# Performance work log

Measured on AMD Instinct MI355X. Metric: run time of the kernel, lower is better.

Reference implementation:

```python
import jax, jax.numpy as jnp
import numpy as np

B, T, D, H, F = 256, 512, 200, 128, 128
LAM = 0.5


def _xavier(key, shape, gain=1.0):
    fan_in, fan_out = shape[0], shape[1]
    lim = gain * np.sqrt(6.0 / (fan_in + fan_out))
    return jax.random.uniform(key, shape, minval=-lim, maxval=lim, dtype=jnp.float32)


def setup_inputs() -> dict:
    key = jax.random.key(0)
    ks = jax.random.split(key, 32)
    inp = {
        "hrrp": jax.random.normal(ks[0], (B, T, D), jnp.float32),
        "amplitude_corr": jax.random.normal(ks[1], (B, T), jnp.float32),
        "phase_corr": jax.random.normal(ks[2], (B, T), jnp.float32),
        "rlos_delta": jax.random.normal(ks[3], (B, T, 2), jnp.float32),
        # TwoStageFusion params (weights stored [in, out])
        "f_amp_w": _xavier(ks[4], (1, F)), "f_amp_b": jnp.zeros((F,)),
        "f_ph_w": _xavier(ks[5], (1, F)), "f_ph_b": jnp.zeros((F,)),
        "f_gate_w": _xavier(ks[6], (2 * F, F)), "f_gate_b": jnp.zeros((F,)),
        "f_rlos_w1": _xavier(ks[7], (2, F)), "f_rlos_b1": jnp.zeros((F,)),
        "f_rlos_w2": _xavier(ks[8], (F, F)), "f_rlos_b2": jnp.zeros((F,)),
        "f_q_w": _xavier(ks[9], (F, F)), "f_q_b": jnp.zeros((F,)),
        "f_k_w": _xavier(ks[10], (F, F)), "f_k_b": jnp.zeros((F,)),
        "f_v_w": _xavier(ks[11], (F, F)), "f_v_b": jnp.zeros((F,)),
        "f_out_w": _xavier(ks[12], (F, F)), "f_out_b": jnp.zeros((F,)),
        # CGLSTM cell params; layer 0 has input_dim=D, layers 1-2 have input_dim=H
        "base_w0": _xavier(ks[13], (D + H, 4 * H)),
        "base_b0": jnp.zeros((4 * H,)).at[H:2 * H].set(1.0),
        "gam_w0": jnp.stack([_xavier(ks[14 + i], (F, H), gain=0.5) for i in range(4)]),
        "base_w12": jnp.stack([_xavier(ks[18 + l], (H + H, 4 * H)) for l in range(2)]),
        "base_b12": jnp.tile(jnp.zeros((4 * H,)).at[H:2 * H].set(1.0)[None], (2, 1)),
        "gam_w12": jnp.stack([jnp.stack([_xavier(ks[20 + 4 * l + i], (F, H), gain=0.5) for i in range(4)]) for l in range(2)]),
        "reg_w": _xavier(ks[28], (H, 2)), "reg_b": jnp.zeros((2,)),
    }
    return inp


def _cell(x, h, c, g, W, b, GW):
    # base linear over concat([h, x]) -> 4 gates; gamma-modulated
    z = jnp.concatenate([h, x], axis=-1) @ W + b
    bi, bf, bc, bo = jnp.split(z, 4, axis=-1)
    i = jax.nn.sigmoid(bi + g @ GW[0])
    f = jax.nn.sigmoid(bf - LAM * (g @ GW[1]))
    ch = jnp.tanh(bc + g @ GW[2])
    o = jax.nn.sigmoid(bo + g @ GW[3])
    c2 = f * c + i * ch
    h2 = o * jnp.tanh(c2)
    return h2, c2


def reference(hrrp, amplitude_corr, phase_corr, rlos_delta,
              f_amp_w, f_amp_b, f_ph_w, f_ph_b, f_gate_w, f_gate_b,
              f_rlos_w1, f_rlos_b1, f_rlos_w2, f_rlos_b2,
              f_q_w, f_q_b, f_k_w, f_k_b, f_v_w, f_v_b, f_out_w, f_out_b,
              base_w0, base_b0, gam_w0, base_w12, base_b12, gam_w12,
              reg_w, reg_b):
    # --- TwoStageFusion ---
    amp = jnp.tanh(amplitude_corr[..., None] @ f_amp_w + f_amp_b)    # [B,T,F]
    ph = jnp.tanh(phase_corr[..., None] @ f_ph_w + f_ph_b)           # [B,T,F]
    beta = jax.nn.sigmoid(jnp.concatenate([ph, amp], -1) @ f_gate_w + f_gate_b)
    corr = beta * ph + (1.0 - beta) * amp
    rl = jnp.tanh(jnp.tanh(rlos_delta @ f_rlos_w1 + f_rlos_b1) @ f_rlos_w2 + f_rlos_b2)
    q = corr @ f_q_w + f_q_b
    k = rl @ f_k_w + f_k_b
    v = rl @ f_v_w + f_v_b
    attn = jax.nn.sigmoid(jnp.sum(q * k, -1, keepdims=True) * (F ** -0.5))
    gamma = (attn * v) @ f_out_w + f_out_b                            # [B,T,F]

    # --- StackedCGLSTM: gamma_t at step t is gamma[:, t-1], zeros at t=0 ---
    gamma_sh = jnp.concatenate([jnp.zeros((gamma.shape[0], 1, gamma.shape[-1]), gamma.dtype),
                                gamma[:, :-1]], axis=1)
    xs = (jnp.swapaxes(hrrp, 0, 1), jnp.swapaxes(gamma_sh, 0, 1))     # [T,B,*]

    bsz = hrrp.shape[0]
    z = jnp.zeros((bsz, H), hrrp.dtype)
    init = ((z, z, z), (z, z, z))

    def step(carry, xt):
        x_t, g_t = xt
        hs, cs = carry
        inp = jnp.abs(x_t)
        h0, c0 = _cell(inp, hs[0], cs[0], g_t, base_w0, base_b0, gam_w0)
        h1, c1 = _cell(h0, hs[1], cs[1], g_t, base_w12[0], base_b12[0], gam_w12[0])
        h2, c2 = _cell(h1, hs[2], cs[2], g_t, base_w12[1], base_b12[1], gam_w12[1])
        return ((h0, h1, h2), (c0, c1, c2)), None

    (hs, _), _ = jax.lax.scan(step, init, xs)
    return hs[2] @ reg_w + reg_b                                      # [B,2]
```

## Files before the change

kernel.cpp:

```cpp
#include <hip/hip_runtime.h>

#define BB 256
#define TT 512
#define DD 200

__device__ __forceinline__ float bf2f(unsigned short u) {
    return __uint_as_float(((unsigned int)u) << 16);
}
__device__ __forceinline__ unsigned short f2bf(float f) {
    unsigned int u = __float_as_uint(f);
    u += 0x7FFFu + ((u >> 16) & 1u);
    return (unsigned short)(u >> 16);
}
__device__ __forceinline__ float sigm(float x) { return 1.0f / (1.0f + __expf(-x)); }
__device__ __forceinline__ float tanh_(float x) { return 1.0f - 2.0f / (__expf(2.0f * x) + 1.0f); }

typedef __bf16 bf16x8 __attribute__((ext_vector_type(8)));
typedef float  f32x4  __attribute__((ext_vector_type(4)));

#define GPAD 20

__device__ __forceinline__ void gll16(const unsigned short* g, unsigned short* l) {
    __builtin_amdgcn_global_load_lds(
        (const __attribute__((address_space(1))) unsigned int*)g,
        (__attribute__((address_space(3))) unsigned int*)l,
        16, 0, 0);
}

#define MAC16(ACCV, BASE, W) do { \
    const float4* _p4 = (const float4*)(BASE); \
    float4 _v0 = _p4[0], _v1 = _p4[1], _v2 = _p4[2], _v3 = _p4[3]; \
    ACCV[0]  = fmaf(_v0.x,(W),ACCV[0]);  ACCV[1]  = fmaf(_v0.y,(W),ACCV[1]); \
    ACCV[2]  = fmaf(_v0.z,(W),ACCV[2]);  ACCV[3]  = fmaf(_v0.w,(W),ACCV[3]); \
    ACCV[4]  = fmaf(_v1.x,(W),ACCV[4]);  ACCV[5]  = fmaf(_v1.y,(W),ACCV[5]); \
    ACCV[6]  = fmaf(_v1.z,(W),ACCV[6]);  ACCV[7]  = fmaf(_v1.w,(W),ACCV[7]); \
    ACCV[8]  = fmaf(_v2.x,(W),ACCV[8]);  ACCV[9]  = fmaf(_v2.y,(W),ACCV[9]); \
    ACCV[10] = fmaf(_v2.z,(W),ACCV[10]); ACCV[11] = fmaf(_v2.w,(W),ACCV[11]); \
    ACCV[12] = fmaf(_v3.x,(W),ACCV[12]); ACCV[13] = fmaf(_v3.y,(W),ACCV[13]); \
    ACCV[14] = fmaf(_v3.z,(W),ACCV[14]); ACCV[15] = fmaf(_v3.w,(W),ACCV[15]); \
} while (0)

#define MAC8(ACCV, BASE, W) do { \
    const float4* _p4 = (const float4*)(BASE); \
    float4 _v0 = _p4[0], _v1 = _p4[1]; \
    ACCV[0] = fmaf(_v0.x,(W),ACCV[0]); ACCV[1] = fmaf(_v0.y,(W),ACCV[1]); \
    ACCV[2] = fmaf(_v0.z,(W),ACCV[2]); ACCV[3] = fmaf(_v0.w,(W),ACCV[3]); \
    ACCV[4] = fmaf(_v1.x,(W),ACCV[4]); ACCV[5] = fmaf(_v1.y,(W),ACCV[5]); \
    ACCV[6] = fmaf(_v1.z,(W),ACCV[6]); ACCV[7] = fmaf(_v1.w,(W),ACCV[7]); \
} while (0)

#define MAC8_2(A1, A2, BASE, W1, W2) do { \
    const float4* _p4 = (const float4*)(BASE); \
    float4 _v0 = _p4[0], _v1 = _p4[1]; \
    A1[0] = fmaf(_v0.x,(W1),A1[0]); A2[0] = fmaf(_v0.x,(W2),A2[0]); \
    A1[1] = fmaf(_v0.y,(W1),A1[1]); A2[1] = fmaf(_v0.y,(W2),A2[1]); \
    A1[2] = fmaf(_v0.z,(W1),A1[2]); A2[2] = fmaf(_v0.z,(W2),A2[2]); \
    A1[3] = fmaf(_v0.w,(W1),A1[3]); A2[3] = fmaf(_v0.w,(W2),A2[3]); \
    A1[4] = fmaf(_v1.x,(W1),A1[4]); A2[4] = fmaf(_v1.x,(W2),A2[4]); \
    A1[5] = fmaf(_v1.y,(W1),A1[5]); A2[5] = fmaf(_v1.y,(W2),A2[5]); \
    A1[6] = fmaf(_v1.z,(W1),A1[6]); A2[6] = fmaf(_v1.z,(W2),A2[6]); \
    A1[7] = fmaf(_v1.w,(W1),A1[7]); A2[7] = fmaf(_v1.w,(W2),A2[7]); \
} while (0)

__global__ __launch_bounds__(256) void k_prep_b(
    const float* __restrict__ w0, const float* __restrict__ gw0,
    const float* __restrict__ w12, const float* __restrict__ gw12,
    unsigned short* __restrict__ b0t, unsigned short* __restrict__ b1t,
    unsigned short* __restrict__ b2t)
{
    const int n = blockIdx.x;
    const int gate = n >> 7, oo = n & 127;
    const float sgn = (gate == 1) ? -0.5f : 1.0f;
    for (int k = threadIdx.x; k < 1056; k += 256) {
        float w; int isLo;
        if (k < 672) {
            int blk = k / 224, col = k - blk * 224;
            w = (col < 200) ? w0[(size_t)(128 + col) * 512 + n] : 0.f;
            isLo = (blk == 1);
        } else {
            int kg = k - 672, blkg = kg >> 7, colg = kg & 127;
            w = sgn * gw0[(size_t)(gate * 128 + colg) * 128 + oo];
            isLo = (blkg == 1);
        }
        unsigned short hi = f2bf(w);
        b0t[(size_t)n * 1056 + k] = isLo ? f2bf(w - bf2f(hi)) : hi;
    }
    for (int l = 0; l < 2; ++l) {
        unsigned short* dst = l ? b2t : b1t;
        for (int k = threadIdx.x; k < 768; k += 256) {
            float w; int isLo;
            if (k < 384) {
                int blk = k >> 7, col = k & 127;
                w = w12[(size_t)(l * 256 + 128 + col) * 512 + n];
                isLo = (blk == 1);
            } else {
                int kg = k - 384, blkg = kg >> 7, colg = kg & 127;
                w = sgn * gw12[(size_t)((l * 4 + gate) * 128 + colg) * 128 + oo];
                isLo = (blkg == 1);
            }
            unsigned short hi = f2bf(w);
            dst[(size_t)n * 768 + k] = isLo ? f2bf(w - bf2f(hi)) : hi;
        }
    }
}

__global__ __launch_bounds__(128) void k_prep_fuse(
    const float* __restrict__ w_q, const float* __restrict__ b_q,
    const float* __restrict__ w_k, const float* __restrict__ b_k,
    const float* __restrict__ w_v, const float* __restrict__ b_v,
    const float* __restrict__ w_o,
    float* __restrict__ GT, float* __restrict__ WVO,
    float* __restrict__ e1, float* __restrict__ e2,
    float* __restrict__ e0, float* __restrict__ bvo)
{
    __shared__ float sk[128], sv[128];
    __shared__ float rtmp[8];
    const int i = blockIdx.x, f = threadIdx.x;
    sk[f] = w_k[(size_t)i * 128 + f];
    sv[f] = w_v[(size_t)i * 128 + f];
    __syncthreads();
    float g = 0.f, wv = 0.f;
    #pragma unroll 4
    for (int a = 0; a < 128; ++a) {
        g  = fmaf(w_q[(size_t)f * 128 + a], sk[a], g);
        wv = fmaf(sv[a], w_o[(size_t)a * 128 + f], wv);
    }
    GT[(size_t)i * 128 + f] = g;
    WVO[(size_t)i * 128 + f] = wv;
    float p1 = w_q[(size_t)i * 128 + f] * b_k[f];
    float p2 = sk[f] * b_q[f];
    #pragma unroll
    for (int sh = 32; sh > 0; sh >>= 1) {
        p1 += __shfl_xor(p1, sh, 64);
        p2 += __shfl_xor(p2, sh, 64);
    }
    if ((f & 63) == 0) { rtmp[(f >> 6) * 2] = p1; rtmp[(f >> 6) * 2 + 1] = p2; }
    __syncthreads();
    if (f == 0) { e1[i] = rtmp[0] + rtmp[2]; e2[i] = rtmp[1] + rtmp[3]; }
    if (i == 0) {
        float bw = 0.f;
        #pragma unroll 4
        for (int a = 0; a < 128; ++a) bw = fmaf(b_v[a], w_o[(size_t)a * 128 + f], bw);
        bvo[f] = bw;
        float p0 = b_q[f] * b_k[f];
        #pragma unroll
        for (int sh = 32; sh > 0; sh >>= 1) p0 += __shfl_xor(p0, sh, 64);
        if ((f & 63) == 0) rtmp[4 + (f >> 6)] = p0;
        __syncthreads();
        if (f == 0) e0[0] = rtmp[4] + rtmp[5];
    }
}

__global__ __launch_bounds__(256, 4) void k_gamma2(
    const float* __restrict__ ac, const float* __restrict__ pc,
    const float* __restrict__ rd,
    const float* __restrict__ w_amp, const float* __restrict__ b_amp,
    const float* __restrict__ w_ph,  const float* __restrict__ b_ph,
    const float* __restrict__ w_g,   const float* __restrict__ b_g,
    const float* __restrict__ w_r1,  const float* __restrict__ b_r1,
    const float* __restrict__ w_r2,  const float* __restrict__ b_r2,
    const float* __restrict__ GT,    const float* __restrict__ WVO,
    const float* __restrict__ e1,    const float* __restrict__ e2,
    const float* __restrict__ e0,    const float* __restrict__ bvo,
    const float* __restrict__ b_o,
    unsigned short* __restrict__ gsh, int segLen, int lgSeg, int tbase)
{
    __shared__ alignas(16) float catT[256][GPAD];
    __shared__ alignas(16) float rlT[128][GPAD];
    __shared__ float scin[4][16];
    __shared__ float red[2][2][8];

    const int tid = threadIdx.x;
    const int f = tid & 127;
    const int th = tid >> 7;
    const int t0 = th * 8;
    const int r0 = blockIdx.x * 16;
    const int b = r0 >> lgSeg;
    const int tl = r0 & (segLen - 1);
    const int tau0 = tbase + tl - 1;

    if (tid < 64) {
        int j = tid >> 4, tt = tid & 15;
        int tau = tau0 + tt; if (tau < 0) tau = 0;
        size_t tok = (size_t)b * TT + tau;
        float v;
        if (j == 0) v = ac[tok];
        else if (j == 1) v = pc[tok];
        else v = rd[tok * 2 + (j - 2)];
        scin[j][tt] = v;
    }
    const float wa = w_amp[f], ba = b_amp[f];
    const float wp = w_ph[f],  bpv = b_ph[f];
    const float w1a = w_r1[f], w1b = w_r1[128 + f];
    const float br1 = b_r1[f], br2v = b_r2[f];
    const float bg = b_g[f];
    __syncthreads();

    float ph8[8], am8[8];
    #pragma unroll
    for (int t = 0; t < 8; ++t) {
        float a = scin[0][t0 + t], p = scin[1][t0 + t];
        float r0v = scin[2][t0 + t], r1v = scin[3][t0 + t];
        float phv = tanh_(fmaf(p, wp, bpv));
        float amv = tanh_(fmaf(a, wa, ba));
        ph8[t] = phv; am8[t] = amv;
        catT[f][t0 + t] = phv;
        catT[128 + f][t0 + t] = amv;
        rlT[f][t0 + t] = tanh_(fmaf(r1v, w1b, fmaf(r0v, w1a, br1)));
    }
    __syncthreads();

    float bacc[8], racc[8];
    #pragma unroll
    for (int t = 0; t < 8; ++t) { bacc[t] = 0.f; racc[t] = 0.f; }
    #pragma unroll 2
    for (int i = 0; i < 128; ++i) {
        float wg1 = w_g[i * 128 + f];
        float wg2 = w_g[(128 + i) * 128 + f];
        float wr  = w_r2[i * 128 + f];
        MAC8(bacc, &catT[i][t0], wg1);
        MAC8(bacc, &catT[128 + i][t0], wg2);
        MAC8(racc, &rlT[i][t0], wr);
    }
    float corr8[8], rl8[8];
    #pragma unroll
    for (int t = 0; t < 8; ++t) {
        float beta = sigm(bacc[t] + bg);
        corr8[t] = fmaf(beta, ph8[t] - am8[t], am8[t]);
        rl8[t] = tanh_(racc[t] + br2v);
    }
    __syncthreads();
    #pragma unroll
    for (int t = 0; t < 8; ++t) rlT[f][t0 + t] = rl8[t];
    __syncthreads();

    float uacc[8], voacc[8];
    #pragma unroll
    for (int t = 0; t < 8; ++t) { uacc[t] = 0.f; voacc[t] = 0.f; }
    #pragma unroll 2
    for (int i = 0; i < 128; ++i) {
        float wu = GT[i * 128 + f];
        float wv = WVO[i * 128 + f];
        MAC8_2(uacc, voacc, &rlT[i][t0], wu, wv);
    }

    const int lane = tid & 63, wv2 = (tid >> 6) & 1;
    const float e1f = e1[f], e2f = e2[f], e0v = e0[0];
    #pragma unroll
    for (int t = 0; t < 8; ++t) {
        float pdot = fmaf(corr8[t], uacc[t] + e1f, rl8[t] * e2f);
        #pragma unroll
        for (int sh = 32; sh > 0; sh >>= 1) pdot += __shfl_xor(pdot, sh, 64);
        if (lane == 0) red[th][wv2][t] = pdot;
    }
    __syncthreads();
    const float bvof = bvo[f], bof = b_o[f];
    #pragma unroll
    for (int t = 0; t < 8; ++t) {
        float attn = sigm((red[th][0][t] + red[th][1][t] + e0v) * 0.088388347648318447f);
        float g = fmaf(attn, voacc[t] + bvof, bof);
        if (tau0 + t0 + t < 0) g = 0.f;
        unsigned short hi = f2bf(g);
        gsh[(size_t)(r0 + t0 + t) * 256 + f] = hi;
        gsh[(size_t)(r0 + t0 + t) * 256 + 128 + f] = f2bf(g - bf2f(hi));
    }
}

__global__ __launch_bounds__(128) void k_gamma(
    const float* __restrict__ ac, const float* __restrict__ pc,
    const float* __restrict__ rd,
    const float* __restrict__ w_amp, const float* __restrict__ b_amp,
    const float* __restrict__ w_ph,  const float* __restrict__ b_ph,
    const float* __restrict__ w_g,   const float* __restrict__ b_g,
    const float* __restrict__ w_r1,  const float* __restrict__ b_r1,
    const float* __restrict__ w_r2,  const float* __restrict__ b_r2,
    const float* __restrict__ w_q,   const float* __restrict__ b_q,
    const float* __restrict__ w_k,   const float* __restrict__ b_k,
    const float* __restrict__ w_v,   const float* __restrict__ b_v,
    const float* __restrict__ w_o,   const float* __restrict__ b_o,
    unsigned short* __restrict__ gsh, int segLen, int lgSeg, int tbase)
{
    __shared__ alignas(16) float catT[256][GPAD];
    __shared__ alignas(16) float rlT[128][GPAD];
    __shared__ alignas(16) float avT[128][GPAD];
    __shared__ float scin[4][16];
    __shared__ float red[2][16];

    const int f = threadIdx.x;
    const int r0 = blockIdx.x * 16;
    const int b = r0 >> lgSeg;
    const int tl = r0 & (segLen - 1);
    const int tau0 = tbase + tl - 1;

    if (f < 64) {
        int j = f >> 4, tt = f & 15;
        int tau = tau0 + tt; if (tau < 0) tau = 0;
        size_t tok = (size_t)b * TT + tau;
        float v;
        if (j == 0) v = ac[tok];
        else if (j == 1) v = pc[tok];
        else v = rd[tok * 2 + (j - 2)];
        scin[j][tt] = v;
    }
    const float wa = w_amp[f], ba = b_amp[f];
    const float wp = w_ph[f],  bpv = b_ph[f];
    const float w1a = w_r1[f], w1b = w_r1[128 + f];
    const float br1 = b_r1[f], br2 = b_r2[f];
    const float bg = b_g[f];
    const float bqv = b_q[f], bkv = b_k[f];
    const float bvv = b_v[f], bov = b_o[f];
    __syncthreads();

    float ph16[16], am16[16];
    #pragma unroll
    for (int t = 0; t < 16; ++t) {
        float a = scin[0][t], p = scin[1][t], r0v = scin[2][t], r1v = scin[3][t];
        float phv = tanh_(fmaf(p, wp, bpv));
        float amv = tanh_(fmaf(a, wa, ba));
        ph16[t] = phv; am16[t] = amv;
        catT[f][t] = phv;
        catT[128 + f][t] = amv;
        rlT[f][t] = tanh_(fmaf(r1v, w1b, fmaf(r0v, w1a, br1)));
    }
    __syncthreads();

    float bacc[16], racc[16];
    #pragma unroll
    for (int t = 0; t < 16; ++t) { bacc[t] = 0.f; racc[t] = 0.f; }
    #pragma unroll 2
    for (int i = 0; i < 128; ++i) {
        float wg1 = w_g[i * 128 + f];
        float wg2 = w_g[(128 + i) * 128 + f];
        float wr  = w_r2[i * 128 + f];
        MAC16(bacc, &catT[i][0], wg1);
        MAC16(bacc, &catT[128 + i][0], wg2);
        MAC16(racc, &rlT[i][0], wr);
    }
    float corr16[16], rl16[16];
    #pragma unroll
    for (int t = 0; t < 16; ++t) {
        float beta = sigm(bacc[t] + bg);
        corr16[t] = fmaf(beta, ph16[t] - am16[t], am16[t]);
        rl16[t] = tanh_(racc[t] + br2);
    }
    __syncthreads();
    #pragma unroll
    for (int t = 0; t < 16; ++t) { catT[f][t] = corr16[t]; rlT[f][t] = rl16[t]; }
    __syncthreads();

    float qa[16], ka[16], va[16];
    #pragma unroll
    for (int t = 0; t < 16; ++t) { qa[t] = 0.f; ka[t] = 0.f; va[t] = 0.f; }
    #pragma unroll 2
    for (int i = 0; i < 128; ++i) {
        float wq = w_q[i * 128 + f];
        float wk = w_k[i * 128 + f];
        float wv = w_v[i * 128 + f];
        MAC16(qa, &catT[i][0], wq);
        MAC16(ka, &rlT[i][0], wk);
        MAC16(va, &rlT[i][0], wv);
    }
    const int lane = f & 63, wvi = f >> 6;
    #pragma unroll
    for (int t = 0; t < 16; ++t) {
        float pdot = (qa[t] + bqv) * (ka[t] + bkv);
        #pragma unroll
        for (int sh = 32; sh > 0; sh >>= 1) pdot += __shfl_xor(pdot, sh, 64);
        if (lane == 0) red[wvi][t] = pdot;
    }
    __syncthreads();
    #pragma unroll
    for (int t = 0; t < 16; ++t) {
        float attn = sigm((red[0][t] + red[1][t]) * 0.088388347648318447f);
        avT[f][t] = attn * (va[t] + bvv);
    }
    __syncthreads();
    float oacc[16];
    #pragma unroll
    for (int t = 0; t < 16; ++t) oacc[t] = 0.f;
    #pragma unroll 2
    for (int i = 0; i < 128; ++i) {
        float wo = w_o[i * 128 + f];
        MAC16(oacc, &avT[i][0], wo);
    }
    #pragma unroll
    for (int t = 0; t < 16; ++t) {
        float g = oacc[t] + bov;
        if (tau0 + t < 0) g = 0.f;
        unsigned short hi = f2bf(g);
        gsh[(size_t)(r0 + t) * 256 + f] = hi;
        gsh[(size_t)(r0 + t) * 256 + 128 + f] = f2bf(g - bf2f(hi));
    }
}

__global__ __launch_bounds__(256) void k_stagex(
    const float* __restrict__ hrrp, unsigned short* __restrict__ xs,
    int segLen, int lgSeg, int tbase)
{
    const int m = blockIdx.x;
    const int b = m >> lgSeg, tl = m & (segLen - 1);
    const size_t bt = (size_t)b * TT + tbase + tl;
    const int col = threadIdx.x;
    if (col < 224) {
        float v = (col < 200) ? fabsf(hrrp[bt * DD + col]) : 0.f;
        unsigned short hi = f2bf(v);
        xs[(size_t)m * 448 + col] = hi;
        xs[(size_t)m * 448 + 224 + col] = f2bf(v - bf2f(hi));
    }
}

template<int KTOT>
__device__ __forceinline__ const unsigned short* addrA(
    const unsigned short* __restrict__ Ax, const unsigned short* __restrict__ Ag,
    int m, int ko)
{
    if (KTOT == 1056) {
        if (ko < 672) {
            int blk = ko / 224, col = ko - blk * 224;
            return Ax + (size_t)m * 448 + (blk == 2 ? 224 : 0) + col;
        }
        int kg = ko - 672, blkg = kg >> 7, colg = kg & 127;
        return Ag + (size_t)m * 256 + (blkg == 2 ? 128 : 0) + colg;
    } else {
        if (ko < 384) {
            int blk = ko >> 7, col = ko & 127;
            return Ax + (size_t)m * 256 + (blk == 2 ? 128 : 0) + col;
        }
        int kg = ko - 384, blkg = kg >> 7, colg = kg & 127;
        return Ag + (size_t)m * 256 + (blkg == 2 ? 128 : 0) + colg;
    }
}

template<int KTOT>
__global__ __launch_bounds__(256) void k_gemm(
    const unsigned short* __restrict__ Ax, const unsigned short* __restrict__ Ag,
    const unsigned short* __restrict__ Bt, const float* __restrict__ bp,
    float* __restrict__ C)
{
    __shared__ alignas(16) unsigned short Als[2][4096];
    __shared__ alignas(16) unsigned short Bls[2][4096];
    const int tid = threadIdx.x;
    const int m0 = blockIdx.x * 128, n0 = blockIdx.y * 128;
    const int wave = tid >> 6, lane = tid & 63;
    const int lm = lane & 15, lq = lane >> 4;
    const int wm = wave >> 1, wn = wave & 1;
    const int srow = tid >> 2, scol = (tid & 3) * 8;
    const int wb = wave * 512;

    const f32x4 vzero = {0.f, 0.f, 0.f, 0.f};
    f32x4 acc[4][4];
    #pragma unroll
    for (int x = 0; x < 4; ++x)
        #pragma unroll
        for (int y = 0; y < 4; ++y) acc[x][y] = vzero;

    float bn[4];
    #pragma unroll
    for (int nt = 0; nt < 4; ++nt) bn[nt] = bp[n0 + wn * 64 + nt * 16 + lm];

    constexpr int NKB = KTOT / 32;

    #define STAGE(buf, kb) do { \
        const int _ko = (kb) * 32 + scol; \
        gll16(addrA<KTOT>(Ax, Ag, m0 + srow, _ko),        &Als[buf][wb]); \
        gll16(addrA<KTOT>(Ax, Ag, m0 + 64 + srow, _ko),   &Als[buf][2048 + wb]); \
        gll16(Bt + (size_t)(n0 + srow) * KTOT + _ko,      &Bls[buf][wb]); \
        gll16(Bt + (size_t)(n0 + 64 + srow) * KTOT + _ko, &Bls[buf][2048 + wb]); \
    } while (0)

    STAGE(0, 0);
    __syncthreads();
    int cur = 0;
    for (int kb = 0; kb < NKB; ++kb) {
        if (kb + 1 < NKB) STAGE(cur ^ 1, kb + 1);
        bf16x8 af[4], bfr[4];
        #pragma unroll
        for (int mt = 0; mt < 4; ++mt)
            af[mt] = *(const bf16x8*)&Als[cur][(wm * 64 + mt * 16 + lm) * 32 + lq * 8];
        #pragma unroll
        for (int nt = 0; nt < 4; ++nt)
            bfr[nt] = *(const bf16x8*)&Bls[cur][(wn * 64 + nt * 16 + lm) * 32 + lq * 8];
        #pragma unroll
        for (int mt = 0; mt < 4; ++mt)
            #pragma unroll
            for (int nt = 0; nt < 4; ++nt)
                acc[mt][nt] = __builtin_amdgcn_mfma_f32_16x16x32_bf16(af[mt], bfr[nt], acc[mt][nt], 0, 0, 0);
        __syncthreads();
        cur ^= 1;
    }
    #undef STAGE

    #pragma unroll
    for (int mt = 0; mt < 4; ++mt) {
        #pragma unroll
        for (int nt = 0; nt < 4; ++nt) {
            const int m = m0 + wm * 64 + mt * 16 + lq * 4;
            const int n = n0 + wn * 64 + nt * 16 + lm;
            #pragma unroll
            for (int r = 0; r < 4; ++r)
                C[(size_t)(m + r) * 512 + n] = acc[mt][nt][r] + bn[nt];
        }
    }
}

template<int STORE_XH, int FINAL>
__global__ __launch_bounds__(1024, 4) void k_scan2(
    const float* __restrict__ pre, const float* __restrict__ Wh,
    float* __restrict__ st_h, float* __restrict__ st_c,
    unsigned short* __restrict__ xh, float* __restrict__ outp,
    const float* __restrict__ regw, const float* __restrict__ regb,
    int first, int R)
{
    const int tid = threadIdx.x;
    const int o = tid & 511;
    const int kh = tid >> 9;
    const int b = blockIdx.x;
    __shared__ alignas(16) float hbuf[128];
    __shared__ float zbuf[1024];

    float wc[64];
    #pragma unroll
    for (int i = 0; i < 64; ++i) wc[i] = Wh[(size_t)(kh * 64 + i) * 512 + o];

    float c = 0.f;
    if (tid < 128) {
        float h0 = 0.f;
        if (!first) { h0 = st_h[b * 128 + tid]; c = st_c[b * 128 + tid]; }
        hbuf[tid] = h0;
    }
    __syncthreads();

    const float* preb = pre + (size_t)b * R * 512;
    float p = (kh == 0) ? preb[o] : 0.f;
    for (int t = 0; t < R; ++t) {
        float q = 0.f;
        if (kh == 0 && t < R - 1) q = preb[(size_t)(t + 1) * 512 + o];
        float acc_a = p, acc_b = 0.f;
        const float* hb = &hbuf[kh * 64];
        #pragma unroll
        for (int i8 = 0; i8 < 8; ++i8) {
            const float4 ha = *(const float4*)&hb[i8 * 8];
            const float4 hc = *(const float4*)&hb[i8 * 8 + 4];
            acc_a = fmaf(ha.x, wc[i8 * 8 + 0], acc_a);
            acc_b = fmaf(hc.x, wc[i8 * 8 + 4], acc_b);
            acc_a = fmaf(ha.y, wc[i8 * 8 + 1], acc_a);
            acc_b = fmaf(hc.y, wc[i8 * 8 + 5], acc_b);
            acc_a = fmaf(ha.z, wc[i8 * 8 + 2], acc_a);
            acc_b = fmaf(hc.z, wc[i8 * 8 + 6], acc_b);
            acc_a = fmaf(ha.w, wc[i8 * 8 + 3], acc_a);
            acc_b = fmaf(hc.w, wc[i8 * 8 + 7], acc_b);
        }
        zbuf[tid] = acc_a + acc_b;
        __syncthreads();
        if (tid < 128) {
            const float zi = zbuf[tid]       + zbuf[512 + tid];
            const float zf = zbuf[tid + 128] + zbuf[512 + tid + 128];
            const float zc = zbuf[tid + 256] + zbuf[512 + tid + 256];
            const float zo = zbuf[tid + 384] + zbuf[512 + tid + 384];
            const float ig = sigm(zi);
            const float fg = sigm(zf);
            const float ch = tanh_(zc);
            const float og = sigm(zo);
            c = fg * c + ig * ch;
            const float h2 = og * tanh_(c);
            hbuf[tid] = h2;
            if (STORE_XH) {
                unsigned short hi = f2bf(h2);
                size_t row = (size_t)b * R + t;
                xh[row * 256 + tid] = hi;
                xh[row * 256 + 128 + tid] = f2bf(h2 - bf2f(hi));
            }
        }
        __syncthreads();
        p = q;
    }
    if (tid < 128) { st_h[b * 128 + tid] = hbuf[tid]; st_c[b * 128 + tid] = c; }
    if (FINAL && tid < 2) {
        float s = regb[tid];
        #pragma unroll 4
        for (int i = 0; i < 128; ++i) s = fmaf(hbuf[i], regw[i * 2 + tid], s);
        outp[b * 2 + tid] = s;
    }
}

extern "C" void kernel_launch(void* const* d_in, const int* in_sizes, int n_in,
                              void* d_out, int out_size, void* d_ws, size_t ws_size,
                              hipStream_t stream)
{
    const float* hrrp = (const float*)d_in[0];
    const float* ac   = (const float*)d_in[1];
    const float* pc   = (const float*)d_in[2];
    const float* rd   = (const float*)d_in[3];
    const float* w_amp= (const float*)d_in[4];
    const float* b_amp= (const float*)d_in[5];
    const float* w_ph = (const float*)d_in[6];
    const float* b_ph = (const float*)d_in[7];
    const float* w_g  = (const float*)d_in[8];
    const float* b_g  = (const float*)d_in[9];
    const float* w_r1 = (const float*)d_in[10];
    const float* b_r1 = (const float*)d_in[11];
    const float* w_r2 = (const float*)d_in[12];
    const float* b_r2 = (const float*)d_in[13];
    const float* w_q  = (const float*)d_in[14];
    const float* b_q  = (const float*)d_in[15];
    const float* w_k  = (const float*)d_in[16];
    const float* b_k  = (const float*)d_in[17];
    const float* w_v  = (const float*)d_in[18];
    const float* b_v  = (const float*)d_in[19];
    const float* w_o  = (const float*)d_in[20];
    const float* b_o  = (const float*)d_in[21];
    const float* w0   = (const float*)d_in[22];
    const float* b0   = (const float*)d_in[23];
    const float* gw0  = (const float*)d_in[24];
    const float* w12  = (const float*)d_in[25];
    const float* b12  = (const float*)d_in[26];
    const float* gw12 = (const float*)d_in[27];
    const float* regw = (const float*)d_in[28];
    const float* regb = (const float*)d_in[29];
    float* outp = (float*)d_out;

    const size_t need64 = 68452352ULL, need32 = 35946496ULL;
    const size_t EXTRA = 132864ULL;
    int R, lg, folded;
    if      (ws_size >= need64 + EXTRA) { R = 64; lg = 6; folded = 1; }
    else if (ws_size >= need64)         { R = 64; lg = 6; folded = 0; }
    else if (ws_size >= need32 + EXTRA) { R = 32; lg = 5; folded = 1; }
    else if (ws_size >= need32)         { R = 32; lg = 5; folded = 0; }
    else return;
    const int NSEG = TT / R;
    const int MR = BB * R;

    char* ws = (char*)d_ws;
    size_t off = 0;
    float* pre = (float*)(ws + off);                   off += (size_t)MR * 512 * 4;
    unsigned short* gsh = (unsigned short*)(ws + off); off += (size_t)MR * 256 * 2;
    unsigned short* xh  = (unsigned short*)(ws + off); off += (size_t)MR * 256 * 2;
    unsigned short* xs  = (unsigned short*)(ws + off); off += (size_t)MR * 448 * 2;
    float* sh0 = (float*)(ws + off); off += 131072;
    float* sc0 = (float*)(ws + off); off += 131072;
    float* sh1 = (float*)(ws + off); off += 131072;
    float* sc1 = (float*)(ws + off); off += 131072;
    float* sh2 = (float*)(ws + off); off += 131072;
    float* sc2 = (float*)(ws + off); off += 131072;
    unsigned short* b0t = (unsigned short*)(ws + off); off += 512 * 1056 * 2;
    unsigned short* b1t = (unsigned short*)(ws + off); off += 512 * 768 * 2;
    unsigned short* b2t = (unsigned short*)(ws + off); off += 512 * 768 * 2;
    float* GT = nullptr; float* WVO = nullptr;
    float* e1p = nullptr; float* e2p = nullptr; float* bvop = nullptr; float* e0p = nullptr;
    if (folded) {
        GT   = (float*)(ws + off); off += 128 * 128 * 4;
        WVO  = (float*)(ws + off); off += 128 * 128 * 4;
        e1p  = (float*)(ws + off); off += 512;
        e2p  = (float*)(ws + off); off += 512;
        bvop = (float*)(ws + off); off += 512;
        e0p  = (float*)(ws + off); off += 256;
    }

    k_prep_b<<<512, 256, 0, stream>>>(w0, gw0, w12, gw12, b0t, b1t, b2t);
    if (folded)
        k_prep_fuse<<<128, 128, 0, stream>>>(w_q, b_q, w_k, b_k, w_v, b_v, w_o,
                                             GT, WVO, e1p, e2p, e0p, bvop);

    for (int seg = 0; seg < NSEG; ++seg) {
        const int first = (seg == 0) ? 1 : 0;
        const int tbase = seg * R;
        if (folded)
            k_gamma2<<<MR / 16, 256, 0, stream>>>(ac, pc, rd, w_amp, b_amp, w_ph, b_ph,
                                                  w_g, b_g, w_r1, b_r1, w_r2, b_r2,
                                                  GT, WVO, e1p, e2p, e0p, bvop, b_o,
                                                  gsh, R, lg, tbase);
        else
            k_gamma<<<MR / 16, 128, 0, stream>>>(ac, pc, rd, w_amp, b_amp, w_ph, b_ph,
                                                 w_g, b_g, w_r1, b_r1, w_r2, b_r2,
                                                 w_q, b_q, w_k, b_k, w_v, b_v, w_o, b_o,
                                                 gsh, R, lg, tbase);
        k_stagex<<<MR, 256, 0, stream>>>(hrrp, xs, R, lg, tbase);
        k_gemm<1056><<<dim3(MR / 128, 4), 256, 0, stream>>>(xs, gsh, b0t, b0, pre);
        k_scan2<1, 0><<<BB, 1024, 0, stream>>>(pre, w0, sh0, sc0, xh,
                                               nullptr, nullptr, nullptr, first, R);
        k_gemm<768><<<dim3(MR / 128, 4), 256, 0, stream>>>(xh, gsh, b1t, b12, pre);
        k_scan2<1, 0><<<BB, 1024, 0, stream>>>(pre, w12, sh1, sc1, xh,
                                               nullptr, nullptr, nullptr, first, R);
        k_gemm<768><<<dim3(MR / 128, 4), 256, 0, stream>>>(xh, gsh, b2t, b12 + 512, pre);
        if (seg < NSEG - 1)
            k_scan2<0, 0><<<BB, 1024, 0, stream>>>(pre, w12 + 256 * 512, sh2, sc2,
                                                   nullptr, nullptr, nullptr, nullptr, first, R);
        else
            k_scan2<0, 1><<<BB, 1024, 0, stream>>>(pre, w12 + 256 * 512, sh2, sc2,
                                                   nullptr, outp, regw, regb, first, R);
    }
}
```

Baseline: 3.177 ms.

## Split recurrent matvec K four ways with two outputs per thread in scan

The recurrent scan kernel now splits the 128-long hidden dot product into four 32-element K slices. Each thread computes two adjacent gate outputs, so every h value read from LDS feeds two FMAs. Partial sums go to a 4x512 LDS buffer and are reduced by the 128 update threads. Those threads also add the precomputed input term and prefetch the next step's pre-activations, instead of kh==0 threads doing it during the matvec. Occupancy is pinned with waves_per_eu(4,4). The serial update phase gains extra LDS reads and a global load on the critical path.

```diff
diff --git a/kernel.cpp b/kernel.cpp
--- a/kernel.cpp
+++ b/kernel.cpp
@@ -504,7 +504,9 @@
 }
 
 template<int STORE_XH, int FINAL>
-__global__ __launch_bounds__(1024, 4) void k_scan2(
+__global__ __launch_bounds__(1024)
+__attribute__((amdgpu_waves_per_eu(4, 4)))
+void k_scan3(
     const float* __restrict__ pre, const float* __restrict__ Wh,
     float* __restrict__ st_h, float* __restrict__ st_c,
     unsigned short* __restrict__ xh, float* __restrict__ outp,
@@ -512,51 +514,55 @@
     int first, int R)
 {
     const int tid = threadIdx.x;
-    const int o = tid & 511;
-    const int kh = tid >> 9;
+    const int i2 = tid & 255;
+    const int kq = tid >> 8;
+    const int o1 = i2 * 2;
     const int b = blockIdx.x;
     __shared__ alignas(16) float hbuf[128];
-    __shared__ float zbuf[1024];
-
-    float wc[64];
-    #pragma unroll
-    for (int i = 0; i < 64; ++i) wc[i] = Wh[(size_t)(kh * 64 + i) * 512 + o];
-
-    float c = 0.f;
+    __shared__ alignas(16) float zbuf[4 * 512];
+
+    float wcA[32], wcB[32];
+    #pragma unroll
+    for (int k = 0; k < 32; ++k) {
+        const float* wp = &Wh[(size_t)(kq * 32 + k) * 512 + o1];
+        wcA[k] = wp[0];
+        wcB[k] = wp[1];
+    }
+
+    const float* preb = pre + (size_t)b * R * 512;
+    float c = 0.f, pv0 = 0.f, pv1 = 0.f, pv2 = 0.f, pv3 = 0.f;
     if (tid < 128) {
         float h0 = 0.f;
         if (!first) { h0 = st_h[b * 128 + tid]; c = st_c[b * 128 + tid]; }
         hbuf[tid] = h0;
-    }
-    __syncthreads();
-
-    const float* preb = pre + (size_t)b * R * 512;
-    float p = (kh == 0) ? preb[o] : 0.f;
+        pv0 = preb[tid];       pv1 = preb[128 + tid];
+        pv2 = preb[256 + tid]; pv3 = preb[384 + tid];
+    }
+    __syncthreads();
+
     for (int t = 0; t < R; ++t) {
-        float q = 0.f;
-        if (kh == 0 && t < R - 1) q = preb[(size_t)(t + 1) * 512 + o];
-        float acc_a = p, acc_b = 0.f;
-        const float* hb = &hbuf[kh * 64];
-        #pragma unroll
-        for (int i8 = 0; i8 < 8; ++i8) {
-            const float4 ha = *(const float4*)&hb[i8 * 8];
-            const float4 hc = *(const float4*)&hb[i8 * 8 + 4];
-            acc_a = fmaf(ha.x, wc[i8 * 8 + 0], acc_a);
-            acc_b = fmaf(hc.x, wc[i8 * 8 + 4], acc_b);
-            acc_a = fmaf(ha.y, wc[i8 * 8 + 1], acc_a);
-            acc_b = fmaf(hc.y, wc[i8 * 8 + 5], acc_b);
-            acc_a = fmaf(ha.z, wc[i8 * 8 + 2], acc_a);
-            acc_b = fmaf(hc.z, wc[i8 * 8 + 6], acc_b);
-            acc_a = fmaf(ha.w, wc[i8 * 8 + 3], acc_a);
-            acc_b = fmaf(hc.w, wc[i8 * 8 + 7], acc_b);
+        float a1 = 0.f, a2 = 0.f;
+        const float* hb = &hbuf[kq * 32];
+        #pragma unroll
+        for (int k8 = 0; k8 < 8; ++k8) {
+            const float4 h4 = *(const float4*)&hb[k8 * 4];
+            a1 = fmaf(h4.x, wcA[k8 * 4 + 0], a1); a2 = fmaf(h4.x, wcB[k8 * 4 + 0], a2);
+            a1 = fmaf(h4.y, wcA[k8 * 4 + 1], a1); a2 = fmaf(h4.y, wcB[k8 * 4 + 1], a2);
+            a1 = fmaf(h4.z, wcA[k8 * 4 + 2], a1); a2 = fmaf(h4.z, wcB[k8 * 4 + 2], a2);
+            a1 = fmaf(h4.w, wcA[k8 * 4 + 3], a1); a2 = fmaf(h4.w, wcB[k8 * 4 + 3], a2);
         }
-        zbuf[tid] = acc_a + acc_b;
+        float2 z2; z2.x = a1; z2.y = a2;
+        *(float2*)&zbuf[kq * 512 + o1] = z2;
         __syncthreads();
         if (tid < 128) {
-            const float zi = zbuf[tid]       + zbuf[512 + tid];
-            const float zf = zbuf[tid + 128] + zbuf[512 + tid + 128];
-            const float zc = zbuf[tid + 256] + zbuf[512 + tid + 256];
-            const float zo = zbuf[tid + 384] + zbuf[512 + tid + 384];
+            const float zi = zbuf[tid]
+                           + zbuf[512 + tid] + zbuf[1024 + tid] + zbuf[1536 + tid] + pv0;
+            const float zf = zbuf[128 + tid]
+                           + zbuf[512 + 128 + tid] + zbuf[1024 + 128 + tid] + zbuf[1536 + 128 + tid] + pv1;
+            const float zc = zbuf[256 + tid]
+                           + zbuf[512 + 256 + tid] + zbuf[1024 + 256 + tid] + zbuf[1536 + 256 + tid] + pv2;
+            const float zo = zbuf[384 + tid]
+                           + zbuf[512 + 384 + tid] + zbuf[1024 + 384 + tid] + zbuf[1536 + 384 + tid] + pv3;
             const float ig = sigm(zi);
             const float fg = sigm(zf);
             const float ch = tanh_(zc);
@@ -570,9 +576,13 @@
                 xh[row * 256 + tid] = hi;
                 xh[row * 256 + 128 + tid] = f2bf(h2 - bf2f(hi));
             }
+            if (t + 1 < R) {
+                const float* pnx = preb + (size_t)(t + 1) * 512;
+                pv0 = pnx[tid];       pv1 = pnx[128 + tid];
+                pv2 = pnx[256 + tid]; pv3 = pnx[384 + tid];
+            }
         }
         __syncthreads();
-        p = q;
     }
     if (tid < 128) { st_h[b * 128 + tid] = hbuf[tid]; st_c[b * 128 + tid] = c; }
     if (FINAL && tid < 2) {
@@ -676,17 +686,17 @@
                                                  gsh, R, lg, tbase);
         k_stagex<<<MR, 256, 0, stream>>>(hrrp, xs, R, lg, tbase);
         k_gemm<1056><<<dim3(MR / 128, 4), 256, 0, stream>>>(xs, gsh, b0t, b0, pre);
-        k_scan2<1, 0><<<BB, 1024, 0, stream>>>(pre, w0, sh0, sc0, xh,
+        k_scan3<1, 0><<<BB, 1024, 0, stream>>>(pre, w0, sh0, sc0, xh,
                                                nullptr, nullptr, nullptr, first, R);
         k_gemm<768><<<dim3(MR / 128, 4), 256, 0, stream>>>(xh, gsh, b1t, b12, pre);
-        k_scan2<1, 0><<<BB, 1024, 0, stream>>>(pre, w12, sh1, sc1, xh,
+        k_scan3<1, 0><<<BB, 1024, 0, stream>>>(pre, w12, sh1, sc1, xh,
                                                nullptr, nullptr, nullptr, first, R);
         k_gemm<768><<<dim3(MR / 128, 4), 256, 0, stream>>>(xh, gsh, b2t, b12 + 512, pre);
         if (seg < NSEG - 1)
-            k_scan2<0, 0><<<BB, 1024, 0, stream>>>(pre, w12 + 256 * 512, sh2, sc2,
+            k_scan3<0, 0><<<BB, 1024, 0, stream>>>(pre, w12 + 256 * 512, sh2, sc2,
                                                    nullptr, nullptr, nullptr, nullptr, first, R);
         else
-            k_scan2<0, 1><<<BB, 1024, 0, stream>>>(pre, w12 + 256 * 512, sh2, sc2,
+            k_scan3<0, 1><<<BB, 1024, 0, stream>>>(pre, w12 + 256 * 512, sh2, sc2,
                                                    nullptr, outp, regw, regb, first, R);
     }
 }
```

Result: faster. 2.754 ms (-13.3%).

## Remap scan threads so gate combine happens in-wave via shuffles, one barrier per step

Applied to the files above, without the earlier changes.

Rewrites the recurrent scan kernel so each wave holds all four gates and both K-halves for eight hidden channels. K-half partial sums and gate activations are now exchanged with cross-lane shuffles instead of through a shared z buffer. The hidden state is double-buffered in LDS, which cuts the per-step barriers from two to one and removes the serial 128-thread gate phase. In exchange every lane computes a transcendental and a redundant cell update, and lanes are mapped to weight columns less contiguously.

```diff
diff --git a/kernel.cpp b/kernel.cpp
--- a/kernel.cpp
+++ b/kernel.cpp
@@ -504,7 +504,9 @@
 }
 
 template<int STORE_XH, int FINAL>
-__global__ __launch_bounds__(1024, 4) void k_scan2(
+__global__ __launch_bounds__(1024)
+__attribute__((amdgpu_waves_per_eu(4, 4)))
+void k_scan5(
     const float* __restrict__ pre, const float* __restrict__ Wh,
     float* __restrict__ st_h, float* __restrict__ st_c,
     unsigned short* __restrict__ xh, float* __restrict__ outp,
@@ -512,73 +514,85 @@
     int first, int R)
 {
     const int tid = threadIdx.x;
-    const int o = tid & 511;
-    const int kh = tid >> 9;
+    const int wave = tid >> 6, lane = tid & 63;
+    const int chl = lane & 7;
+    const int gate = (lane >> 3) & 3;
+    const int kh = lane >> 5;
+    const int ch = wave * 8 + chl;
+    const int o = gate * 128 + ch;
     const int b = blockIdx.x;
-    __shared__ alignas(16) float hbuf[128];
-    __shared__ float zbuf[1024];
+
+    __shared__ alignas(16) float hbuf[2][128];
 
     float wc[64];
     #pragma unroll
-    for (int i = 0; i < 64; ++i) wc[i] = Wh[(size_t)(kh * 64 + i) * 512 + o];
-
-    float c = 0.f;
-    if (tid < 128) {
-        float h0 = 0.f;
-        if (!first) { h0 = st_h[b * 128 + tid]; c = st_c[b * 128 + tid]; }
-        hbuf[tid] = h0;
-    }
-    __syncthreads();
+    for (int k = 0; k < 64; ++k)
+        wc[k] = Wh[(size_t)(kh * 64 + k) * 512 + o];
 
     const float* preb = pre + (size_t)b * R * 512;
-    float p = (kh == 0) ? preb[o] : 0.f;
+    float pv = preb[o];
+    float c = 0.f, hlast = 0.f;
+    if (!first) c = st_c[b * 128 + ch];
+    if (lane < 8) {
+        float h0 = first ? 0.f : st_h[b * 128 + ch];
+        hbuf[0][ch] = h0;
+    }
+    __syncthreads();
+
     for (int t = 0; t < R; ++t) {
-        float q = 0.f;
-        if (kh == 0 && t < R - 1) q = preb[(size_t)(t + 1) * 512 + o];
-        float acc_a = p, acc_b = 0.f;
-        const float* hb = &hbuf[kh * 64];
-        #pragma unroll
-        for (int i8 = 0; i8 < 8; ++i8) {
-            const float4 ha = *(const float4*)&hb[i8 * 8];
-            const float4 hc = *(const float4*)&hb[i8 * 8 + 4];
-            acc_a = fmaf(ha.x, wc[i8 * 8 + 0], acc_a);
-            acc_b = fmaf(hc.x, wc[i8 * 8 + 4], acc_b);
-            acc_a = fmaf(ha.y, wc[i8 * 8 + 1], acc_a);
-            acc_b = fmaf(hc.y, wc[i8 * 8 + 5], acc_b);
-            acc_a = fmaf(ha.z, wc[i8 * 8 + 2], acc_a);
-            acc_b = fmaf(hc.z, wc[i8 * 8 + 6], acc_b);
-            acc_a = fmaf(ha.w, wc[i8 * 8 + 3], acc_a);
-            acc_b = fmaf(hc.w, wc[i8 * 8 + 7], acc_b);
+        const int rb = t & 1;
+        const float* hb = &hbuf[rb][kh * 64];
+        float a0 = 0.f, a1 = 0.f;
+        #pragma unroll
+        for (int k8 = 0; k8 < 8; ++k8) {
+            const float4 h4 = *(const float4*)&hb[k8 * 8];
+            const float4 h5 = *(const float4*)&hb[k8 * 8 + 4];
+            a0 = fmaf(h4.x, wc[k8 * 8 + 0], a0);
+            a1 = fmaf(h5.x, wc[k8 * 8 + 4], a1);
+            a0 = fmaf(h4.y, wc[k8 * 8 + 1], a0);
+            a1 = fmaf(h5.y, wc[k8 * 8 + 5], a1);
+            a0 = fmaf(h4.z, wc[k8 * 8 + 2], a0);
+            a1 = fmaf(h5.z, wc[k8 * 8 + 6], a1);
+            a0 = fmaf(h4.w, wc[k8 * 8 + 3], a0);
+            a1 = fmaf(h5.w, wc[k8 * 8 + 7], a1);
         }
-        zbuf[tid] = acc_a + acc_b;
-        __syncthreads();
-        if (tid < 128) {
-            const float zi = zbuf[tid]       + zbuf[512 + tid];
-            const float zf = zbuf[tid + 128] + zbuf[512 + tid + 128];
-            const float zc = zbuf[tid + 256] + zbuf[512 + tid + 256];
-            const float zo = zbuf[tid + 384] + zbuf[512 + tid + 384];
-            const float ig = sigm(zi);
-            const float fg = sigm(zf);
-            const float ch = tanh_(zc);
-            const float og = sigm(zo);
-            c = fg * c + ig * ch;
-            const float h2 = og * tanh_(c);
-            hbuf[tid] = h2;
-            if (STORE_XH) {
-                unsigned short hi = f2bf(h2);
-                size_t row = (size_t)b * R + t;
-                xh[row * 256 + tid] = hi;
-                xh[row * 256 + 128 + tid] = f2bf(h2 - bf2f(hi));
-            }
+        float z = a0 + a1;
+        z += __shfl_xor(z, 32, 64);
+        z += pv;
+        if (t + 1 < R) pv = preb[(size_t)(t + 1) * 512 + o];
+
+        const bool isc = (gate == 2);
+        const float s = isc ? (z + z) : z;
+        const float e = __expf(s);
+        const float act = 1.f - (isc ? 2.f : 1.f) / (e + 1.f);
+
+        const float v8  = __shfl_xor(act, 8, 64);
+        const float v16 = __shfl_xor(act, 16, 64);
+        const float v24 = __shfl_xor(v8, 16, 64);
+        const int g0 = gate & 1, g1 = gate >> 1;
+        const float ig = g1 ? (g0 ? v24 : v16) : (g0 ? v8  : act);
+        const float fg = g1 ? (g0 ? v16 : v24) : (g0 ? act : v8);
+        const float cg = g1 ? (g0 ? v8  : act) : (g0 ? v24 : v16);
+        const float og = g1 ? (g0 ? act : v8)  : (g0 ? v16 : v24);
+
+        c = fg * c + ig * cg;
+        const float h2 = og * tanh_(c);
+        hlast = h2;
+        if (lane < 8) hbuf[rb ^ 1][ch] = h2;
+        if (STORE_XH && kh == 0 && gate < 2) {
+            unsigned short hi = f2bf(h2);
+            size_t row = (size_t)b * R + t;
+            if (gate == 0) xh[row * 256 + ch] = hi;
+            else           xh[row * 256 + 128 + ch] = f2bf(h2 - bf2f(hi));
         }
         __syncthreads();
-        p = q;
-    }
-    if (tid < 128) { st_h[b * 128 + tid] = hbuf[tid]; st_c[b * 128 + tid] = c; }
+    }
+    if (lane < 8) { st_h[b * 128 + ch] = hlast; st_c[b * 128 + ch] = c; }
     if (FINAL && tid < 2) {
+        const float* hf = &hbuf[R & 1][0];
         float s = regb[tid];
         #pragma unroll 4
-        for (int i = 0; i < 128; ++i) s = fmaf(hbuf[i], regw[i * 2 + tid], s);
+        for (int i = 0; i < 128; ++i) s = fmaf(hf[i], regw[i * 2 + tid], s);
         outp[b * 2 + tid] = s;
     }
 }
@@ -676,17 +690,17 @@
                                                  gsh, R, lg, tbase);
         k_stagex<<<MR, 256, 0, stream>>>(hrrp, xs, R, lg, tbase);
         k_gemm<1056><<<dim3(MR / 128, 4), 256, 0, stream>>>(xs, gsh, b0t, b0, pre);
-        k_scan2<1, 0><<<BB, 1024, 0, stream>>>(pre, w0, sh0, sc0, xh,
+        k_scan5<1, 0><<<BB, 1024, 0, stream>>>(pre, w0, sh0, sc0, xh,
                                                nullptr, nullptr, nullptr, first, R);
         k_gemm<768><<<dim3(MR / 128, 4), 256, 0, stream>>>(xh, gsh, b1t, b12, pre);
-        k_scan2<1, 0><<<BB, 1024, 0, stream>>>(pre, w12, sh1, sc1, xh,
+        k_scan5<1, 0><<<BB, 1024, 0, stream>>>(pre, w12, sh1, sc1, xh,
                                                nullptr, nullptr, nullptr, first, R);
         k_gemm<768><<<dim3(MR / 128, 4), 256, 0, stream>>>(xh, gsh, b2t, b12 + 512, pre);
         if (seg < NSEG - 1)
-            k_scan2<0, 0><<<BB, 1024, 0, stream>>>(pre, w12 + 256 * 512, sh2, sc2,
+            k_scan5<0, 0><<<BB, 1024, 0, stream>>>(pre, w12 + 256 * 512, sh2, sc2,
                                                    nullptr, nullptr, nullptr, nullptr, first, R);
         else
-            k_scan2<0, 1><<<BB, 1024, 0, stream>>>(pre, w12 + 256 * 512, sh2, sc2,
+            k_scan5<0, 1><<<BB, 1024, 0, stream>>>(pre, w12 + 256 * 512, sh2, sc2,
                                                    nullptr, outp, regw, regb, first, R);
     }
 }
```

After: 2.985 ms. -6.0%, faster.
